# Kernel tuning notes

Measured on AMD Instinct MI355X. Metric: run time of the kernel, lower is better.

The kernel has to match this reference:

```python
import jax, jax.numpy as jnp
import numpy as np

N_CVS = 4096
FEAT = 128
BATCH = 8192
K = 15
EPSILON = 0.9
E_MIN = 0.9 ** 10


def setup_inputs() -> dict:
    key = jax.random.key(0)
    k1, k2, k3 = jax.random.split(key, 3)
    x = jax.random.normal(k1, (BATCH, FEAT), dtype=jnp.float32)
    labels = jax.random.randint(k2, (BATCH,), 0, N_CVS, dtype=jnp.int64 if jax.config.jax_enable_x64 else jnp.int32)
    cvs = jax.random.normal(k3, (N_CVS, FEAT), dtype=jnp.float32)
    # module state buffers: identity-initialized edge / connectedness matrices
    edges = jnp.eye(N_CVS, dtype=jnp.float32)
    cv_connectedness = jnp.eye(N_CVS, dtype=jnp.float32)
    return {"x": x, "cvs": cvs, "edges": edges, "cv_connectedness": cv_connectedness, "labels": labels}


def reference(x, cvs, edges, cv_connectedness, labels):
    B = x.shape[0]
    N = cvs.shape[0]
    # squared pairwise distances (same ordering as cdist; x_cvs = cdist**2)
    d2 = (jnp.sum(x * x, axis=1)[:, None]
          + jnp.sum(cvs * cvs, axis=1)[None, :]
          - 2.0 * (x @ cvs.T))
    d2 = jnp.maximum(d2, 0.0)  # [B, N]

    # k nearest codevectors per sample (smallest distance first)
    _, knn = jax.lax.top_k(-d2, K)        # [B, K]
    closest = knn[:, 0]                    # [B]

    # visits per codevector (Counter over closest)
    visits = jnp.zeros((N,), dtype=jnp.float32).at[closest].add(1.0)
    # encounters[i, j] = visits[i]
    encounters = jnp.broadcast_to(visits[:, None], (N, N))

    # closest_cv_encounters[closest[i], knn[i, k]] += 1
    rows = jnp.repeat(closest, K)
    cols = knn.reshape(-1)
    cce = jnp.zeros((N, N), dtype=jnp.float32).at[rows, cols].add(1.0)

    existence = cce > 0
    enc = jnp.maximum(encounters - cce, 0.0)

    # edge update (state): refresh visited edges, exponentially decay others
    edges_new = jnp.maximum(edges, existence.astype(edges.dtype))
    edges_new = edges_new * (EPSILON ** enc)
    edges_new = jnp.where(edges_new < E_MIN, 0.0, edges_new)

    # margin loss
    d_pos = jnp.sum((x - cvs[labels]) ** 2, axis=1)                  # [B]
    neigh_mask = (edges_new > 0) & (cv_connectedness < 1)            # [N, N]
    d_neg = d2 * neigh_mask[labels].astype(d2.dtype)                 # [B, N]
    e_neg = jnp.exp(-0.001 * d_neg) * (d_neg > 0)
    w = e_neg / jnp.sum(e_neg, axis=1, keepdims=True)
    w = jnp.where(jnp.isnan(w), 0.0, w)
    w = jax.lax.stop_gradient(w)
    mu = d_pos - jnp.sum(w * d_neg, axis=1)
    loss = jnp.sum(jnp.maximum(mu, 0.0)) / B
    return loss
```

## Files before the change

### kernel.cpp

```cpp
#include <hip/hip_runtime.h>
#include <math.h>

#define N_CVS   4096
#define FEAT    128
#define BATCH   8192
#define KNN_K   15
#define E_MIN_F 0.34867844f

typedef __attribute__((ext_vector_type(8))) short bf16x8;
typedef __attribute__((ext_vector_type(4))) float f32x4;

__global__ void norms_kernel(const float* __restrict__ x, const float* __restrict__ cvs,
                             float* __restrict__ x2, float* __restrict__ c2) {
    int wid  = blockIdx.x * 4 + (threadIdx.x >> 6);
    int lane = threadIdx.x & 63;
    const float* src; float* dst;
    if (wid < BATCH) { src = x + (size_t)wid * FEAT; dst = x2 + wid; }
    else             { int r = wid - BATCH; src = cvs + (size_t)r * FEAT; dst = c2 + r; }
    float2 v = ((const float2*)src)[lane];
    float s = v.x * v.x + v.y * v.y;
    #pragma unroll
    for (int off = 32; off > 0; off >>= 1) s += __shfl_xor(s, off, 64);
    if (lane == 0) *dst = s;
}

__global__ void cvt_kernel(const float* __restrict__ x, const float* __restrict__ cvs,
                           unsigned short* __restrict__ xb, unsigned short* __restrict__ cb) {
    size_t f = ((size_t)blockIdx.x * 256 + threadIdx.x) * 8;
    const float* src; unsigned short* dst;
    if (f < (size_t)BATCH * FEAT) { src = x + f; dst = xb + f; }
    else { size_t g = f - (size_t)BATCH * FEAT; src = cvs + g; dst = cb + g; }
    float4 v0 = ((const float4*)src)[0];
    float4 v1 = ((const float4*)src)[1];
    float vv[8] = {v0.x, v0.y, v0.z, v0.w, v1.x, v1.y, v1.z, v1.w};
    bf16x8 o;
    #pragma unroll
    for (int i = 0; i < 8; ++i) {
        unsigned u = __float_as_uint(vv[i]);
        o[i] = (short)((u + 0x7fffu + ((u >> 16) & 1u)) >> 16);
    }
    *(bf16x8*)dst = o;
}

#define LROW 272
__global__ __launch_bounds__(256) void mfma_d2_kernel(
        const unsigned short* __restrict__ xb, const unsigned short* __restrict__ cb,
        const float* __restrict__ x2g, const float* __restrict__ c2g,
        float* __restrict__ d2) {
    __shared__ __align__(16) char lds[2 * 128 * LROW];
    char* Al = lds;
    char* Bl = lds + 128 * LROW;
    const int bi = blockIdx.y * 128;
    const int bj = blockIdx.x * 128;
    const int t  = threadIdx.x;

    #pragma unroll
    for (int i = 0; i < 8; ++i) {
        int f = t + i * 256;
        int row = f >> 4, g = f & 15;
        ulonglong2 va = *(const ulonglong2*)((const char*)(xb + (size_t)(bi + row) * FEAT) + g * 16);
        *(ulonglong2*)(Al + row * LROW + g * 16) = va;
        ulonglong2 vb = *(const ulonglong2*)((const char*)(cb + (size_t)(bj + row) * FEAT) + g * 16);
        *(ulonglong2*)(Bl + row * LROW + g * 16) = vb;
    }
    __syncthreads();

    const int lane = t & 63;
    const int wave = t >> 6;
    const int wr = (wave >> 1) * 64;
    const int wc = (wave & 1) * 64;
    const int l15 = lane & 15, quad = lane >> 4;

    f32x4 acc[4][4];
    #pragma unroll
    for (int i = 0; i < 4; ++i)
        #pragma unroll
        for (int j = 0; j < 4; ++j)
            acc[i][j] = (f32x4){0.f, 0.f, 0.f, 0.f};

    #pragma unroll
    for (int ks = 0; ks < 4; ++ks) {
        bf16x8 a[4], b[4];
        #pragma unroll
        for (int s = 0; s < 4; ++s) {
            a[s] = *(const bf16x8*)(Al + (wr + s * 16 + l15) * LROW + ks * 64 + quad * 16);
            b[s] = *(const bf16x8*)(Bl + (wc + s * 16 + l15) * LROW + ks * 64 + quad * 16);
        }
        #pragma unroll
        for (int si = 0; si < 4; ++si)
            #pragma unroll
            for (int sj = 0; sj < 4; ++sj)
                acc[si][sj] = __builtin_amdgcn_mfma_f32_16x16x32_bf16(a[si], b[sj], acc[si][sj], 0, 0, 0);
    }

    #pragma unroll
    for (int si = 0; si < 4; ++si) {
        #pragma unroll
        for (int r = 0; r < 4; ++r) {
            int m = bi + wr + si * 16 + quad * 4 + r;
            float xv = x2g[m];
            float* orow = d2 + (size_t)m * N_CVS + bj + wc;
            #pragma unroll
            for (int sj = 0; sj < 4; ++sj) {
                int nloc = sj * 16 + l15;
                float v = xv + c2g[bj + wc + nloc] - 2.0f * acc[si][sj][r];
                orow[nloc] = fmaxf(v, 0.0f);
            }
        }
    }
}

__global__ __launch_bounds__(256) void topk_kernel(const float* __restrict__ d2,
                                                   int* __restrict__ knn) {
    __shared__ unsigned long long cand[4][64];
    const int wv   = threadIdx.x >> 6;
    const int wid  = blockIdx.x * 4 + wv;
    const int lane = threadIdx.x & 63;
    const float* row = d2 + (size_t)wid * N_CVS;

    float4 v[16];
    #pragma unroll
    for (int i = 0; i < 16; ++i)
        v[i] = *(const float4*)(row + lane * 4 + i * 256);

    float mn = fminf(fminf(v[0].x, v[0].y), fminf(v[0].z, v[0].w));
    #pragma unroll
    for (int i = 1; i < 16; ++i)
        mn = fminf(mn, fminf(fminf(v[i].x, v[i].y), fminf(v[i].z, v[i].w)));

    float s = mn;
    #pragma unroll
    for (int k = 2; k <= 64; k <<= 1) {
        #pragma unroll
        for (int j = k >> 1; j > 0; j >>= 1) {
            float o = __shfl_xor(s, j, 64);
            bool lower = ((lane & j) == 0);
            bool asc   = ((lane & k) == 0);
            float lo = fminf(s, o), hi = fmaxf(s, o);
            s = (lower == asc) ? lo : hi;
        }
    }
    float T = __shfl(s, 15, 64);

    unsigned long long* cbuf = cand[wv];
    int base = 0;
    #pragma unroll
    for (int i = 0; i < 16; ++i) {
        float vv[4] = {v[i].x, v[i].y, v[i].z, v[i].w};
        #pragma unroll
        for (int c = 0; c < 4; ++c) {
            bool p = (vv[c] <= T);
            unsigned long long mask = __ballot(p);
            if (p) {
                int pos = base + __popcll(mask & ((1ULL << lane) - 1ULL));
                if (pos < 64)
                    cbuf[pos] = ((unsigned long long)__float_as_uint(vv[c]) << 32)
                              | (unsigned)(lane * 4 + i * 256 + c);
            }
            base += __popcll(mask);
        }
    }
    __builtin_amdgcn_wave_barrier();

    int* outp = knn + wid * KNN_K;
    if (base <= 64) {
        unsigned long long key = (lane < base) ? cbuf[lane] : ~0ULL;
        for (int r = 0; r < KNN_K; ++r) {
            unsigned long long m = key;
            #pragma unroll
            for (int off = 32; off > 0; off >>= 1) {
                unsigned long long o = __shfl_xor(m, off, 64);
                m = (o < m) ? o : m;
            }
            if (lane == 0) outp[r] = (int)(unsigned)(m & 0xffffffffu);
            if (key == m) key = ~0ULL;
        }
    } else {
        unsigned long long heap[15];
        #pragma unroll
        for (int k = 0; k < 15; ++k) heap[k] = ~0ULL;
        for (int i = 0; i < 16; ++i) {
            int j0 = lane * 4 + i * 256;
            float4 f4 = *(const float4*)(row + j0);
            float vv[4] = {f4.x, f4.y, f4.z, f4.w};
            #pragma unroll
            for (int c = 0; c < 4; ++c) {
                unsigned long long key =
                    ((unsigned long long)__float_as_uint(vv[c]) << 32) | (unsigned)(j0 + c);
                if (key < heap[14]) {
                    heap[14] = key;
                    #pragma unroll
                    for (int k = 14; k > 0; --k) {
                        unsigned long long a = heap[k-1], b = heap[k];
                        bool sw = b < a;
                        heap[k-1] = sw ? b : a;
                        heap[k]   = sw ? a : b;
                    }
                }
            }
        }
        for (int r = 0; r < KNN_K; ++r) {
            unsigned long long cd = heap[0];
            unsigned long long m = cd;
            #pragma unroll
            for (int off = 32; off > 0; off >>= 1) {
                unsigned long long o = __shfl_xor(m, off, 64);
                m = (o < m) ? o : m;
            }
            if (lane == 0) outp[r] = (int)(unsigned)(m & 0xffffffffu);
            if (cd == m) {
                #pragma unroll
                for (int k = 0; k < 14; ++k) heap[k] = heap[k+1];
                heap[14] = ~0ULL;
            }
        }
    }
}

__global__ void scatter_kernel(const int* __restrict__ knn, int* __restrict__ visits,
                               int* __restrict__ cce) {
    int b = blockIdx.x * 256 + threadIdx.x;
    const int* kr = knn + b * KNN_K;
    int closest = kr[0];
    atomicAdd(&visits[closest], 1);
    size_t base = (size_t)closest * N_CVS;
    #pragma unroll
    for (int k = 0; k < KNN_K; ++k) atomicAdd(&cce[base + kr[k]], 1);
}

__global__ void bits_kernel(const int* __restrict__ cce, const int* __restrict__ visits,
                            const float* __restrict__ edges, const float* __restrict__ conn,
                            unsigned long long* __restrict__ bits) {
    size_t idx = (size_t)blockIdx.x * 256 + threadIdx.x;
    int i = (int)(idx >> 12);
    int cc = cce[idx];
    float e = edges[idx];
    float ex = fmaxf(e, cc > 0 ? 1.0f : 0.0f);
    bool pass = false;
    if (ex > 0.0f) {
        float enc = fmaxf((float)visits[i] - (float)cc, 0.0f);
        float en = ex * powf(0.9f, enc);
        pass = (en >= E_MIN_F) && (conn[idx] < 1.0f);
    }
    unsigned long long bal = __ballot(pass);
    if ((threadIdx.x & 63) == 0) bits[idx >> 6] = bal;
}

__global__ void loss_kernel(const float* __restrict__ d2,
                            const unsigned long long* __restrict__ bits,
                            const int* __restrict__ labels, float* __restrict__ partial) {
    int wid  = blockIdx.x * 4 + (threadIdx.x >> 6);
    int lane = threadIdx.x & 63;
    int l = labels[wid];
    const unsigned long long* rb = bits + (size_t)l * 64;
    const float* row = d2 + (size_t)wid * N_CVS;
    float se = 0.f, sed = 0.f;
    unsigned long long w = rb[lane];
    while (w) {
        int c = __builtin_ctzll(w);
        w &= w - 1;
        int j = lane * 64 + c;
        float d = row[j];
        if (d > 0.f) {
            float ee = __expf(-0.001f * d);
            se += ee; sed += ee * d;
        }
    }
    #pragma unroll
    for (int off = 32; off > 0; off >>= 1) {
        se  += __shfl_xor(se,  off, 64);
        sed += __shfl_xor(sed, off, 64);
    }
    if (lane == 0) {
        float dpos = row[l];
        float wsum = se > 0.f ? sed / se : 0.f;
        float mu = dpos - wsum;
        partial[wid] = (mu > 0.f) ? mu : 0.f;
    }
}

__global__ void reduce_kernel(const float* __restrict__ partial, float* __restrict__ out) {
    int t = threadIdx.x;
    float s = 0.f;
    #pragma unroll
    for (int i = 0; i < BATCH / 256; ++i) s += partial[t + i * 256];
    #pragma unroll
    for (int off = 32; off > 0; off >>= 1) s += __shfl_xor(s, off, 64);
    __shared__ float wsum[4];
    if ((t & 63) == 0) wsum[t >> 6] = s;
    __syncthreads();
    if (t == 0) out[0] = (wsum[0] + wsum[1] + wsum[2] + wsum[3]) * (1.0f / BATCH);
}

extern "C" void kernel_launch(void* const* d_in, const int* in_sizes, int n_in,
                              void* d_out, int out_size, void* d_ws, size_t ws_size,
                              hipStream_t stream) {
    const float* x      = (const float*)d_in[0];
    const float* cvs    = (const float*)d_in[1];
    const float* edges  = (const float*)d_in[2];
    const float* conn   = (const float*)d_in[3];
    const int*   labels = (const int*)d_in[4];

    char* p = (char*)d_ws;
    float* d2 = (float*)p;                  p += (size_t)BATCH * N_CVS * 4;
    int* knn  = (int*)p;                    p += (size_t)BATCH * KNN_K * 4;
    int* visits = (int*)p;                  p += (size_t)N_CVS * 4;
    int* cce  = (int*)p;                    p += (size_t)N_CVS * N_CVS * 4;
    unsigned long long* bits = (unsigned long long*)p;
                                            p += (size_t)N_CVS * 64 * 8;
    float* x2 = (float*)p;                  p += (size_t)BATCH * 4;
    float* c2 = (float*)p;                  p += (size_t)N_CVS * 4;
    unsigned short* xb = (unsigned short*)p; p += (size_t)BATCH * FEAT * 2;
    unsigned short* cb = (unsigned short*)p; p += (size_t)N_CVS * FEAT * 2;
    float* partial = (float*)p;             p += (size_t)BATCH * 4;

    hipMemsetAsync(visits, 0, (size_t)N_CVS * 4 + (size_t)N_CVS * N_CVS * 4, stream);

    norms_kernel  <<<(BATCH + N_CVS) / 4, 256, 0, stream>>>(x, cvs, x2, c2);
    cvt_kernel    <<<(BATCH + N_CVS) * FEAT / 8 / 256, 256, 0, stream>>>(x, cvs, xb, cb);
    mfma_d2_kernel<<<dim3(N_CVS / 128, BATCH / 128), 256, 0, stream>>>(xb, cb, x2, c2, d2);
    topk_kernel   <<<BATCH / 4, 256, 0, stream>>>(d2, knn);
    scatter_kernel<<<BATCH / 256, 256, 0, stream>>>(knn, visits, cce);
    bits_kernel   <<<(size_t)N_CVS * N_CVS / 256, 256, 0, stream>>>(cce, visits, edges, conn, bits);
    loss_kernel   <<<BATCH / 4, 256, 0, stream>>>(d2, bits, labels, partial);
    reduce_kernel <<<1, 256, 0, stream>>>(partial, (float*)d_out);
}
```

Before: 259.4 us.

## Pack cce counts into bytes and vectorize bits kernel with float4 loads

The co-encounter count matrix is stored as 8-bit counters packed four per word and updated with shifted atomic adds, which cuts the memset and the read traffic for the N×N matrix by a factor of four. The bits kernel now handles four columns per thread using float4 loads of edges and connectedness. It rebuilds the 64-bit masks by interleaving four ballots with a bit-spread routine, and replaces powf with __expf. The cost is a risk of 8-bit overflow if a single cell were hit 256 or more times, plus slightly different exp rounding near the threshold.

```diff
diff --git a/kernel.cpp b/kernel.cpp
--- a/kernel.cpp
+++ b/kernel.cpp
@@ -6,6 +6,7 @@
 #define BATCH   8192
 #define KNN_K   15
 #define E_MIN_F 0.34867844f
+#define LN09    -0.105360516f
 
 typedef __attribute__((ext_vector_type(8))) short bf16x8;
 typedef __attribute__((ext_vector_type(4))) float f32x4;
@@ -218,32 +219,67 @@
 }
 
 __global__ void scatter_kernel(const int* __restrict__ knn, int* __restrict__ visits,
-                               int* __restrict__ cce) {
+                               unsigned int* __restrict__ cce8) {
     int b = blockIdx.x * 256 + threadIdx.x;
     const int* kr = knn + b * KNN_K;
     int closest = kr[0];
     atomicAdd(&visits[closest], 1);
     size_t base = (size_t)closest * N_CVS;
     #pragma unroll
-    for (int k = 0; k < KNN_K; ++k) atomicAdd(&cce[base + kr[k]], 1);
-}
-
-__global__ void bits_kernel(const int* __restrict__ cce, const int* __restrict__ visits,
-                            const float* __restrict__ edges, const float* __restrict__ conn,
-                            unsigned long long* __restrict__ bits) {
-    size_t idx = (size_t)blockIdx.x * 256 + threadIdx.x;
-    int i = (int)(idx >> 12);
-    int cc = cce[idx];
-    float e = edges[idx];
-    float ex = fmaxf(e, cc > 0 ? 1.0f : 0.0f);
-    bool pass = false;
-    if (ex > 0.0f) {
-        float enc = fmaxf((float)visits[i] - (float)cc, 0.0f);
-        float en = ex * powf(0.9f, enc);
-        pass = (en >= E_MIN_F) && (conn[idx] < 1.0f);
-    }
-    unsigned long long bal = __ballot(pass);
-    if ((threadIdx.x & 63) == 0) bits[idx >> 6] = bal;
+    for (int k = 0; k < KNN_K; ++k) {
+        size_t idx = base + kr[k];
+        atomicAdd((int*)&cce8[idx >> 2], 1 << ((idx & 3) * 8));
+    }
+}
+
+__device__ inline unsigned long long spread4(unsigned long long x) {
+    x = (x | (x << 24)) & 0x000000ff000000ffULL;
+    x = (x | (x << 12)) & 0x000f000f000f000fULL;
+    x = (x | (x << 6))  & 0x0303030303030303ULL;
+    x = (x | (x << 3))  & 0x1111111111111111ULL;
+    return x;
+}
+
+__global__ __launch_bounds__(256) void bits_kernel(
+        const unsigned int* __restrict__ cce8, const int* __restrict__ visits,
+        const float4* __restrict__ edges, const float4* __restrict__ conn,
+        unsigned long long* __restrict__ bits) {
+    size_t tid = (size_t)blockIdx.x * 256 + threadIdx.x;
+    int i = (int)(tid >> 10);
+    float vis = (float)visits[i];
+    unsigned cw = cce8[tid];
+    float4 ev = edges[tid];
+    float4 cv = conn[tid];
+    float ea[4] = {ev.x, ev.y, ev.z, ev.w};
+    float ca[4] = {cv.x, cv.y, cv.z, cv.w};
+    bool p[4];
+    #pragma unroll
+    for (int c = 0; c < 4; ++c) {
+        int cc = (cw >> (c * 8)) & 0xff;
+        float e = ea[c];
+        float ex = (cc > 0) ? fmaxf(e, 1.0f) : e;
+        bool pass = false;
+        if (ex > 0.0f) {
+            float enc = fmaxf(vis - (float)cc, 0.0f);
+            float en = ex * __expf(enc * LN09);
+            pass = (en >= E_MIN_F) && (ca[c] < 1.0f);
+        }
+        p[c] = pass;
+    }
+    unsigned long long b0 = __ballot(p[0]);
+    unsigned long long b1 = __ballot(p[1]);
+    unsigned long long b2 = __ballot(p[2]);
+    unsigned long long b3 = __ballot(p[3]);
+    int lane = threadIdx.x & 63;
+    int wv   = threadIdx.x >> 6;
+    if (lane < 4) {
+        int sh = lane * 16;
+        unsigned long long w = spread4((b0 >> sh) & 0xffff)
+                             | (spread4((b1 >> sh) & 0xffff) << 1)
+                             | (spread4((b2 >> sh) & 0xffff) << 2)
+                             | (spread4((b3 >> sh) & 0xffff) << 3);
+        bits[(size_t)blockIdx.x * 16 + wv * 4 + lane] = w;
+    }
 }
 
 __global__ void loss_kernel(const float* __restrict__ d2,
@@ -305,7 +341,7 @@
     float* d2 = (float*)p;                  p += (size_t)BATCH * N_CVS * 4;
     int* knn  = (int*)p;                    p += (size_t)BATCH * KNN_K * 4;
     int* visits = (int*)p;                  p += (size_t)N_CVS * 4;
-    int* cce  = (int*)p;                    p += (size_t)N_CVS * N_CVS * 4;
+    unsigned int* cce8 = (unsigned int*)p;  p += (size_t)N_CVS * N_CVS;
     unsigned long long* bits = (unsigned long long*)p;
                                             p += (size_t)N_CVS * 64 * 8;
     float* x2 = (float*)p;                  p += (size_t)BATCH * 4;
@@ -314,14 +350,15 @@
     unsigned short* cb = (unsigned short*)p; p += (size_t)N_CVS * FEAT * 2;
     float* partial = (float*)p;             p += (size_t)BATCH * 4;
 
-    hipMemsetAsync(visits, 0, (size_t)N_CVS * 4 + (size_t)N_CVS * N_CVS * 4, stream);
+    hipMemsetAsync(visits, 0, (size_t)N_CVS * 4 + (size_t)N_CVS * N_CVS, stream);
 
     norms_kernel  <<<(BATCH + N_CVS) / 4, 256, 0, stream>>>(x, cvs, x2, c2);
     cvt_kernel    <<<(BATCH + N_CVS) * FEAT / 8 / 256, 256, 0, stream>>>(x, cvs, xb, cb);
     mfma_d2_kernel<<<dim3(N_CVS / 128, BATCH / 128), 256, 0, stream>>>(xb, cb, x2, c2, d2);
     topk_kernel   <<<BATCH / 4, 256, 0, stream>>>(d2, knn);
-    scatter_kernel<<<BATCH / 256, 256, 0, stream>>>(knn, visits, cce);
-    bits_kernel   <<<(size_t)N_CVS * N_CVS / 256, 256, 0, stream>>>(cce, visits, edges, conn, bits);
+    scatter_kernel<<<BATCH / 256, 256, 0, stream>>>(knn, visits, cce8);
+    bits_kernel   <<<(size_t)N_CVS * N_CVS / 4 / 256, 256, 0, stream>>>(
+                      cce8, visits, (const float4*)edges, (const float4*)conn, bits);
     loss_kernel   <<<BATCH / 4, 256, 0, stream>>>(d2, bits, labels, partial);
     reduce_kernel <<<1, 256, 0, stream>>>(partial, (float*)d_out);
 }
```

After: 238.6 us. 8.0% less time.

## Pack encounter counts into bytes, vectorize edge-bit kernel, fuse norms into conversion

Applied to the files above, without the earlier changes.

The co-encounter count matrix shrinks from int32 to packed 8-bit counters, updated through shifted atomic adds on 32-bit words. This cuts the memset and the bits-kernel read traffic by a factor of four. The bits kernel now has each thread handle 16 consecutive entries with vector loads, and uses a closed-form threshold check in place of powf. The norm computation is also folded into the bf16 conversion kernel, which removes one launch and one pass over the inputs. The risk is byte counters overflowing into neighbouring bytes if one pair reaches 256 encounters, which is possible with 8192 samples if a codevector is very popular.

```diff
diff --git a/kernel.cpp b/kernel.cpp
--- a/kernel.cpp
+++ b/kernel.cpp
@@ -6,40 +6,37 @@
 #define BATCH   8192
 #define KNN_K   15
 #define E_MIN_F 0.34867844f
+#define LN09    -0.105360516f
 
 typedef __attribute__((ext_vector_type(8))) short bf16x8;
 typedef __attribute__((ext_vector_type(4))) float f32x4;
 
-__global__ void norms_kernel(const float* __restrict__ x, const float* __restrict__ cvs,
-                             float* __restrict__ x2, float* __restrict__ c2) {
-    int wid  = blockIdx.x * 4 + (threadIdx.x >> 6);
-    int lane = threadIdx.x & 63;
-    const float* src; float* dst;
-    if (wid < BATCH) { src = x + (size_t)wid * FEAT; dst = x2 + wid; }
-    else             { int r = wid - BATCH; src = cvs + (size_t)r * FEAT; dst = c2 + r; }
-    float2 v = ((const float2*)src)[lane];
-    float s = v.x * v.x + v.y * v.y;
-    #pragma unroll
-    for (int off = 32; off > 0; off >>= 1) s += __shfl_xor(s, off, 64);
-    if (lane == 0) *dst = s;
-}
-
-__global__ void cvt_kernel(const float* __restrict__ x, const float* __restrict__ cvs,
-                           unsigned short* __restrict__ xb, unsigned short* __restrict__ cb) {
-    size_t f = ((size_t)blockIdx.x * 256 + threadIdx.x) * 8;
-    const float* src; unsigned short* dst;
-    if (f < (size_t)BATCH * FEAT) { src = x + f; dst = xb + f; }
-    else { size_t g = f - (size_t)BATCH * FEAT; src = cvs + g; dst = cb + g; }
+__global__ void cvtnorm_kernel(const float* __restrict__ x, const float* __restrict__ cvs,
+                               unsigned short* __restrict__ xb, unsigned short* __restrict__ cb,
+                               float* __restrict__ x2, float* __restrict__ c2) {
+    size_t tid = (size_t)blockIdx.x * 256 + threadIdx.x;
+    size_t f = tid * 8;
+    const float* src; unsigned short* dst; float* ndst; size_t row;
+    if (f < (size_t)BATCH * FEAT) { src = x + f; dst = xb + f; row = f >> 7; ndst = x2 + row; }
+    else {
+        size_t g = f - (size_t)BATCH * FEAT;
+        src = cvs + g; dst = cb + g; row = g >> 7; ndst = c2 + row;
+    }
     float4 v0 = ((const float4*)src)[0];
     float4 v1 = ((const float4*)src)[1];
     float vv[8] = {v0.x, v0.y, v0.z, v0.w, v1.x, v1.y, v1.z, v1.w};
     bf16x8 o;
+    float s = 0.f;
     #pragma unroll
     for (int i = 0; i < 8; ++i) {
         unsigned u = __float_as_uint(vv[i]);
         o[i] = (short)((u + 0x7fffu + ((u >> 16) & 1u)) >> 16);
+        s += vv[i] * vv[i];
     }
     *(bf16x8*)dst = o;
+    #pragma unroll
+    for (int off = 1; off < 16; off <<= 1) s += __shfl_xor(s, off, 64);
+    if ((threadIdx.x & 15) == 0) *ndst = s;
 }
 
 #define LROW 272
@@ -218,32 +215,54 @@
 }
 
 __global__ void scatter_kernel(const int* __restrict__ knn, int* __restrict__ visits,
-                               int* __restrict__ cce) {
+                               unsigned int* __restrict__ cce8) {
     int b = blockIdx.x * 256 + threadIdx.x;
     const int* kr = knn + b * KNN_K;
     int closest = kr[0];
     atomicAdd(&visits[closest], 1);
     size_t base = (size_t)closest * N_CVS;
     #pragma unroll
-    for (int k = 0; k < KNN_K; ++k) atomicAdd(&cce[base + kr[k]], 1);
-}
-
-__global__ void bits_kernel(const int* __restrict__ cce, const int* __restrict__ visits,
-                            const float* __restrict__ edges, const float* __restrict__ conn,
-                            unsigned long long* __restrict__ bits) {
-    size_t idx = (size_t)blockIdx.x * 256 + threadIdx.x;
-    int i = (int)(idx >> 12);
-    int cc = cce[idx];
-    float e = edges[idx];
-    float ex = fmaxf(e, cc > 0 ? 1.0f : 0.0f);
-    bool pass = false;
-    if (ex > 0.0f) {
-        float enc = fmaxf((float)visits[i] - (float)cc, 0.0f);
-        float en = ex * powf(0.9f, enc);
-        pass = (en >= E_MIN_F) && (conn[idx] < 1.0f);
-    }
-    unsigned long long bal = __ballot(pass);
-    if ((threadIdx.x & 63) == 0) bits[idx >> 6] = bal;
+    for (int k = 0; k < KNN_K; ++k) {
+        size_t idx = base + kr[k];
+        atomicAdd((int*)&cce8[idx >> 2], 1 << ((idx & 3) * 8));
+    }
+}
+
+__global__ __launch_bounds__(256) void bits_kernel(
+        const uint4* __restrict__ cce8, const int* __restrict__ visits,
+        const float4* __restrict__ edges, const float4* __restrict__ conn,
+        unsigned short* __restrict__ bits16) {
+    const int row = blockIdx.x;
+    const int t   = threadIdx.x;
+    const int vis = visits[row];
+    size_t fb = (size_t)row * 1024 + t * 4;
+    float4 e0 = edges[fb+0], e1 = edges[fb+1], e2 = edges[fb+2], e3 = edges[fb+3];
+    float4 c0 = conn [fb+0], c1 = conn [fb+1], c2_ = conn[fb+2], c3 = conn[fb+3];
+    uint4 cw = cce8[(size_t)row * 256 + t];
+    float ea[16] = {e0.x,e0.y,e0.z,e0.w, e1.x,e1.y,e1.z,e1.w,
+                    e2.x,e2.y,e2.z,e2.w, e3.x,e3.y,e3.z,e3.w};
+    float ca[16] = {c0.x,c0.y,c0.z,c0.w, c1.x,c1.y,c1.z,c1.w,
+                    c2_.x,c2_.y,c2_.z,c2_.w, c3.x,c3.y,c3.z,c3.w};
+    unsigned cwa[4] = {cw.x, cw.y, cw.z, cw.w};
+    unsigned m = 0;
+    #pragma unroll
+    for (int c = 0; c < 16; ++c) {
+        int cc = (cwa[c >> 2] >> ((c & 3) * 8)) & 0xff;
+        float e = ea[c];
+        float ex = (cc > 0) ? fmaxf(e, 1.0f) : e;
+        bool pass;
+        if (ex >= 1.0f) {
+            pass = (vis - cc) <= 10;
+        } else if (ex > 0.0f) {
+            float enc = fmaxf((float)(vis - cc), 0.0f);
+            pass = ex * __expf(enc * LN09) >= E_MIN_F;
+        } else {
+            pass = false;
+        }
+        pass = pass && (ca[c] < 1.0f);
+        m |= (unsigned)pass << c;
+    }
+    bits16[(size_t)row * 256 + t] = (unsigned short)m;
 }
 
 __global__ void loss_kernel(const float* __restrict__ d2,
@@ -305,7 +324,7 @@
     float* d2 = (float*)p;                  p += (size_t)BATCH * N_CVS * 4;
     int* knn  = (int*)p;                    p += (size_t)BATCH * KNN_K * 4;
     int* visits = (int*)p;                  p += (size_t)N_CVS * 4;
-    int* cce  = (int*)p;                    p += (size_t)N_CVS * N_CVS * 4;
+    unsigned int* cce8 = (unsigned int*)p;  p += (size_t)N_CVS * N_CVS;
     unsigned long long* bits = (unsigned long long*)p;
                                             p += (size_t)N_CVS * 64 * 8;
     float* x2 = (float*)p;                  p += (size_t)BATCH * 4;
@@ -314,14 +333,15 @@
     unsigned short* cb = (unsigned short*)p; p += (size_t)N_CVS * FEAT * 2;
     float* partial = (float*)p;             p += (size_t)BATCH * 4;
 
-    hipMemsetAsync(visits, 0, (size_t)N_CVS * 4 + (size_t)N_CVS * N_CVS * 4, stream);
-
-    norms_kernel  <<<(BATCH + N_CVS) / 4, 256, 0, stream>>>(x, cvs, x2, c2);
-    cvt_kernel    <<<(BATCH + N_CVS) * FEAT / 8 / 256, 256, 0, stream>>>(x, cvs, xb, cb);
+    hipMemsetAsync(visits, 0, (size_t)N_CVS * 4 + (size_t)N_CVS * N_CVS, stream);
+
+    cvtnorm_kernel<<<(BATCH + N_CVS) * FEAT / 8 / 256, 256, 0, stream>>>(x, cvs, xb, cb, x2, c2);
     mfma_d2_kernel<<<dim3(N_CVS / 128, BATCH / 128), 256, 0, stream>>>(xb, cb, x2, c2, d2);
     topk_kernel   <<<BATCH / 4, 256, 0, stream>>>(d2, knn);
-    scatter_kernel<<<BATCH / 256, 256, 0, stream>>>(knn, visits, cce);
-    bits_kernel   <<<(size_t)N_CVS * N_CVS / 256, 256, 0, stream>>>(cce, visits, edges, conn, bits);
+    scatter_kernel<<<BATCH / 256, 256, 0, stream>>>(knn, visits, cce8);
+    bits_kernel   <<<N_CVS, 256, 0, stream>>>(
+                      (const uint4*)cce8, visits, (const float4*)edges, (const float4*)conn,
+                      (unsigned short*)bits);
     loss_kernel   <<<BATCH / 4, 256, 0, stream>>>(d2, bits, labels, partial);
     reduce_kernel <<<1, 256, 0, stream>>>(partial, (float*)d_out);
 }
```

Measured after the change: 237.6 us. -8.4%, faster.
